# Optimization experiments

Hardware: AMD Instinct MI355X
Metric: run time of the kernel (lower is better)

Reference implementation:

```python
import jax, jax.numpy as jnp
import numpy as np

Q, M, KLEN, B = 512, 512, 1024, 4
D, H, DH, G = 1024, 16, 64, 4
DG = D // G          # 256
EPS = 1e-6
SCALE = 1.0 / DH ** 0.5


def _group_ln(x, gamma, beta, n_group):
    # x: [L, B, D]; torch std is unbiased (ddof=1); note (x-mean)/(std+eps)
    L, b, d = x.shape
    xg = x.reshape(L, b, n_group, d // n_group)
    mean = xg.mean(-1, keepdims=True)
    std = jnp.std(xg, axis=-1, ddof=1, keepdims=True)
    out = ((xg - mean) / (std + EPS)).reshape(L, b, d)
    return gamma * out + beta


def _rel_shift(x):
    # x: [q, r, b, n]
    q, r = x.shape[0], x.shape[1]
    zero_pad = jnp.zeros((q, 1) + x.shape[2:], x.dtype)
    x_padded = jnp.concatenate([zero_pad, x], axis=1).reshape((r + 1, q) + x.shape[2:])
    return x_padded[1:].reshape(x.shape)


def setup_inputs() -> dict:
    key = jax.random.key(0)
    ks = jax.random.split(key, 14)
    p = lambda k, s: jax.random.normal(k, s, jnp.float32) * 0.02
    w = jax.random.normal(ks[0], (Q, B, D), jnp.float32)
    r = jax.random.normal(ks[1], (KLEN, 1, D), jnp.float32)
    mems = jax.random.normal(ks[2], (M, B, D), jnp.float32)
    r_w_bias = p(ks[3], (H, DH))
    r_r_bias = p(ks[4], (H, DH))
    gamma_q = jnp.ones((D,), jnp.float32); beta_q = jnp.zeros((D,), jnp.float32)
    gamma_kv = jnp.ones((D,), jnp.float32); beta_kv = jnp.zeros((D,), jnp.float32)
    Wq = p(ks[5], (G, DG, DG))       # grouped conv1d k=1: per-group [out,in]
    Wiq = p(ks[6], (DG, D))          # inter_q_net: conv1d groups=1 [out,in]
    Wk = p(ks[7], (D, D))
    Wv = p(ks[8], (D, D))
    Wr = p(ks[9], (G, DG, DG))       # r_net grouped (n_head*d_head == d_model)
    Wintra = p(ks[10], (G, DG, DG))  # intra_linear grouped conv
    Winter = p(ks[11], (DG, D))      # inter_linear nn.Linear weight
    i = jnp.arange(Q)[:, None]
    j = jnp.arange(KLEN)[None, :]
    attn_mask = (j > i + M)[:, :, None]  # [Q, KLEN, 1] bool, True = masked
    return dict(w=w, r=r, r_w_bias=r_w_bias, r_r_bias=r_r_bias, mems=mems,
                gamma_q=gamma_q, beta_q=beta_q, gamma_kv=gamma_kv, beta_kv=beta_kv,
                Wq=Wq, Wiq=Wiq, Wk=Wk, Wv=Wv, Wr=Wr, Wintra=Wintra, Winter=Winter,
                attn_mask=attn_mask)


def reference(w, r, r_w_bias, r_r_bias, mems, gamma_q, beta_q, gamma_kv, beta_kv,
              Wq, Wiq, Wk, Wv, Wr, Wintra, Winter, attn_mask):
    qlen, bsz, _ = w.shape
    rlen = r.shape[0]
    w_norm = _group_ln(w, gamma_q, beta_q, G)                       # [Q,B,D]
    kv = jnp.concatenate([mems, w], axis=0)
    kv_norm = gamma_kv * (kv - kv.mean(-1, keepdims=True)) / (
        jnp.std(kv, axis=-1, ddof=1, keepdims=True) + EPS) + beta_kv  # [K,B,D]

    # grouped 1x1 conv projections == per-group matmuls
    q_intra = jnp.einsum('qbgd,god->qbgo', w_norm.reshape(qlen, bsz, G, DG), Wq)
    q_global = jnp.einsum('qbd,od->qbo', w_norm, Wiq)               # [Q,B,DG]
    head_q = (q_intra + q_global[:, :, None, :]).reshape(qlen, bsz, H, DH)
    klen = kv_norm.shape[0]
    head_k = jnp.einsum('kbd,od->kbo', kv_norm, Wk).reshape(klen, bsz, H, DH)
    head_v = jnp.einsum('kbd,od->kbo', kv_norm, Wv).reshape(klen, bsz, H, DH)
    r_head_k = jnp.einsum('rgd,god->rgo', r[:, 0].reshape(rlen, G, DG), Wr)
    r_head_k = r_head_k.reshape(rlen, H, DH)                        # [R,H,DH]

    AC = jnp.einsum('ibnd,jbnd->ijbn', head_q + r_w_bias, head_k)
    BD = _rel_shift(jnp.einsum('ibnd,jnd->ijbn', head_q + r_r_bias, r_head_k))
    attn_score = (AC + BD) * SCALE                                  # [Q,K,B,H]
    attn_score = jnp.where(attn_mask[:, :, :, None], -jnp.inf, attn_score)
    attn_prob = jax.nn.softmax(attn_score, axis=1)
    attn_vec = jnp.einsum('ijbn,jbnd->ibnd', attn_prob, head_v)
    attn_out = attn_vec.reshape(qlen, bsz, D)

    inter = jnp.einsum('qbd,od->qbo', attn_out, Winter)             # [Q,B,DG]
    intra = jnp.einsum('qbgd,god->qbgo', attn_out.reshape(qlen, bsz, G, DG), Wintra)
    out = (intra + inter[:, :, None, :]).reshape(qlen, bsz, D)
    return w + out
```

## Files before the change

kernel.cpp:

```cpp
#include <hip/hip_runtime.h>
#include <math.h>

#define Q_LEN 512
#define M_LEN 512
#define KL    1024
#define BSZ   4
#define DM    1024
#define NH    16
#define DHD   64
#define NG    4
#define DGRP  256
#define RL    1024
#define LN_EPS 1e-6f
#define ATT_SCALE 0.125f

typedef short s16x8 __attribute__((ext_vector_type(8)));
typedef float f32x4 __attribute__((ext_vector_type(4)));

__device__ __forceinline__ float wave_sum64(float v) {
#pragma unroll
    for (int off = 32; off > 0; off >>= 1) v += __shfl_xor(v, off);
    return v;
}

__device__ __forceinline__ ushort f2bf(float f) {
    unsigned u = __float_as_uint(f);
    unsigned r = (u + 0x7fffu + ((u >> 16) & 1u)) >> 16;
    return (ushort)r;
}
__device__ __forceinline__ float bf2f(ushort u) {
    return __uint_as_float(((unsigned)u) << 16);
}

__global__ __launch_bounds__(256) void prep_kernel(
    const float* __restrict__ r, const float* __restrict__ Wk,
    const float* __restrict__ Wv, const float* __restrict__ Wr,
    const float* __restrict__ Wq, const float* __restrict__ Wiq,
    const float* __restrict__ Wintra, const float* __restrict__ Winter,
    ushort* __restrict__ r_bf, ushort* __restrict__ Wk_bf,
    ushort* __restrict__ Wv_bf, ushort* __restrict__ Wr_bf,
    ushort* __restrict__ Wq_aug, ushort* __restrict__ Wo_aug)
{
    int bid = blockIdx.x;
    if (bid < 3328) {
        const float* s; ushort* d; int off;
        if      (bid < 1024) { s = r;  d = r_bf;  off = bid; }
        else if (bid < 2048) { s = Wk; d = Wk_bf; off = bid - 1024; }
        else if (bid < 3072) { s = Wv; d = Wv_bf; off = bid - 2048; }
        else                 { s = Wr; d = Wr_bf; off = bid - 3072; }
        int i = off * 1024 + threadIdx.x * 4;
        float4 v = *(const float4*)(s + i);
        ushort4 o;
        o.x = f2bf(v.x); o.y = f2bf(v.y); o.z = f2bf(v.z); o.w = f2bf(v.w);
        *(ushort4*)(d + i) = o;
    } else {
        const float* Wg; const float* Wf; ushort* Wo; int off;
        if (bid < 4352) { Wg = Wq;     Wf = Wiq;    Wo = Wq_aug; off = bid - 3328; }
        else            { Wg = Wintra; Wf = Winter; Wo = Wo_aug; off = bid - 4352; }
        int idx = off * 1024 + threadIdx.x * 4;
        int g = idx >> 18;
        int o = (idx >> 10) & 255;
        int k = idx & 1023;
        float4 v = *(const float4*)(Wf + o * 1024 + k);
        if ((k >> 8) == g) {
            float4 vg = *(const float4*)(Wg + ((g * 256 + o) << 8) + (k & 255));
            v.x += vg.x; v.y += vg.y; v.z += vg.z; v.w += vg.w;
        }
        ushort4 u;
        u.x = f2bf(v.x); u.y = f2bf(v.y); u.z = f2bf(v.z); u.w = f2bf(v.w);
        *(ushort4*)(Wo + idx) = u;
    }
}

__global__ __launch_bounds__(64) void group_ln_kernel(
    const float* __restrict__ w, const float* __restrict__ gamma,
    const float* __restrict__ beta, ushort* __restrict__ out)
{
    int bid = blockIdx.x;
    int g = bid & (NG - 1);
    long long row = bid >> 2;
    int t = threadIdx.x;
    long long base = row * DM + g * DGRP + t * 4;
    float4 x = *(const float4*)(w + base);
    float mean = wave_sum64(x.x + x.y + x.z + x.w) * (1.0f / 256.0f);
    float dx = x.x - mean, dy = x.y - mean, dz = x.z - mean, dw = x.w - mean;
    float ss = wave_sum64(dx * dx + dy * dy + dz * dz + dw * dw);
    float inv = 1.0f / (sqrtf(ss * (1.0f / 255.0f)) + LN_EPS);
    int db = g * DGRP + t * 4;
    float4 ga = *(const float4*)(gamma + db);
    float4 be = *(const float4*)(beta + db);
    ushort4 o;
    o.x = f2bf(ga.x * (dx * inv) + be.x);
    o.y = f2bf(ga.y * (dy * inv) + be.y);
    o.z = f2bf(ga.z * (dz * inv) + be.z);
    o.w = f2bf(ga.w * (dw * inv) + be.w);
    *(ushort4*)(out + base) = o;
}

__global__ __launch_bounds__(256) void kv_ln_kernel(
    const float* __restrict__ mems, const float* __restrict__ w,
    const float* __restrict__ gamma, const float* __restrict__ beta,
    ushort* __restrict__ out)
{
    int row = blockIdx.x;
    int k = row >> 2, b = row & 3;
    const float* src = (k < M_LEN) ? (mems + ((long long)k * BSZ + b) * DM)
                                   : (w + ((long long)(k - M_LEN) * BSZ + b) * DM);
    int t = threadIdx.x;
    float4 x = *(const float4*)(src + t * 4);
    __shared__ float red[4];
    float s = wave_sum64(x.x + x.y + x.z + x.w);
    int wv = t >> 6, ln = t & 63;
    if (ln == 0) red[wv] = s;
    __syncthreads();
    float mean = (red[0] + red[1] + red[2] + red[3]) * (1.0f / 1024.0f);
    float dx = x.x - mean, dy = x.y - mean, dz = x.z - mean, dw = x.w - mean;
    float ss = wave_sum64(dx * dx + dy * dy + dz * dz + dw * dw);
    __syncthreads();
    if (ln == 0) red[wv] = ss;
    __syncthreads();
    float var = (red[0] + red[1] + red[2] + red[3]) * (1.0f / 1023.0f);
    float inv = 1.0f / (sqrtf(var) + LN_EPS);
    int db = t * 4;
    float4 ga = *(const float4*)(gamma + db);
    float4 be = *(const float4*)(beta + db);
    ushort4 o;
    o.x = f2bf(ga.x * (dx * inv) + be.x);
    o.y = f2bf(ga.y * (dy * inv) + be.y);
    o.z = f2bf(ga.z * (dz * inv) + be.z);
    o.w = f2bf(ga.w * (dw * inv) + be.w);
    *(ushort4*)(out + (long long)row * DM + db) = o;
}

__global__ __launch_bounds__(256) void gemm128_bf16_nt(
    const ushort* __restrict__ A, int lda,
    const ushort* __restrict__ W, long long wZ, int ldw,
    ushort* __restrict__ Cb, long long cZ, int ldc, int K)
{
    int z = blockIdx.z;
    W += (long long)z * wZ;
    Cb += (long long)z * cZ;
    int m0 = blockIdx.y * 128, n0 = blockIdx.x * 128;
    int t = threadIdx.x, lane = t & 63, w = t >> 6;
    int wr = w >> 1, wc = w & 1;
    int fr = lane & 15, kq = (lane >> 4) * 8;
    int srow = t >> 1, scol = (t & 1) * 16;

    __shared__ __align__(16) ushort As[128][40];
    __shared__ __align__(16) ushort Ws[128][40];

    const ushort* Ar = A + (long long)(m0 + srow) * lda + scol;
    const ushort* Wr = W + (long long)(n0 + srow) * ldw + scol;

    f32x4 acc[16] = {};

    s16x8 a0 = *(const s16x8*)Ar, a1 = *(const s16x8*)(Ar + 8);
    s16x8 b0 = *(const s16x8*)Wr, b1 = *(const s16x8*)(Wr + 8);
    *(s16x8*)&As[srow][scol] = a0; *(s16x8*)&As[srow][scol + 8] = a1;
    *(s16x8*)&Ws[srow][scol] = b0; *(s16x8*)&Ws[srow][scol + 8] = b1;
    __syncthreads();

    for (int k0 = 0; k0 < K; k0 += 32) {
        bool more = (k0 + 32) < K;
        if (more) {
            a0 = *(const s16x8*)(Ar + k0 + 32); a1 = *(const s16x8*)(Ar + k0 + 40);
            b0 = *(const s16x8*)(Wr + k0 + 32); b1 = *(const s16x8*)(Wr + k0 + 40);
        }
        s16x8 af[4], bf_[4];
#pragma unroll
        for (int rb = 0; rb < 4; ++rb)
            af[rb] = *(const s16x8*)&As[wr * 64 + rb * 16 + fr][kq];
#pragma unroll
        for (int cb = 0; cb < 4; ++cb)
            bf_[cb] = *(const s16x8*)&Ws[wc * 64 + cb * 16 + fr][kq];
#pragma unroll
        for (int rb = 0; rb < 4; ++rb)
#pragma unroll
            for (int cb = 0; cb < 4; ++cb)
                acc[rb * 4 + cb] = __builtin_amdgcn_mfma_f32_16x16x32_bf16(
                    af[rb], bf_[cb], acc[rb * 4 + cb], 0, 0, 0);
        __syncthreads();
        if (more) {
            *(s16x8*)&As[srow][scol] = a0; *(s16x8*)&As[srow][scol + 8] = a1;
            *(s16x8*)&Ws[srow][scol] = b0; *(s16x8*)&Ws[srow][scol + 8] = b1;
            __syncthreads();
        }
    }

    int rbase = (lane >> 4) * 4;
#pragma unroll
    for (int rb = 0; rb < 4; ++rb)
#pragma unroll
        for (int p = 0; p < 4; ++p) {
            long long row = m0 + wr * 64 + rb * 16 + rbase + p;
            ushort* crow = Cb + row * ldc + n0 + wc * 64 + fr;
#pragma unroll
            for (int cb = 0; cb < 4; ++cb)
                crow[cb * 16] = f2bf(acc[rb * 4 + cb][p]);
        }
}

__global__ __launch_bounds__(256) void gemm_bf16_nt(
    const ushort* __restrict__ A, long long aZ, int lda,
    const ushort* __restrict__ W, long long wZ, int ldw,
    float* __restrict__ C, ushort* __restrict__ Cb, long long cZ, int ldc,
    int M, int N, int K,
    const float* __restrict__ add1, long long a1Z, int lda1,
    const float* __restrict__ add2, long long a2Z, int lda2)
{
    int z = blockIdx.z;
    A += (long long)z * aZ;
    W += (long long)z * wZ;
    if (C)  C += (long long)z * cZ;
    if (Cb) Cb += (long long)z * cZ;
    if (add1) add1 += (long long)z * a1Z;
    if (add2) add2 += (long long)z * a2Z;
    int m0 = blockIdx.y * 64, n0 = blockIdx.x * 64;
    int t = threadIdx.x;
    int lane = t & 63, wid = t >> 6;
    int wr = wid >> 1, wc = wid & 1;
    int srow = t >> 2, scol = (t & 3) * 16;
    int fr = lane & 15, kq = (lane >> 4) * 8;

    __shared__ __align__(16) ushort As[64][72];
    __shared__ __align__(16) ushort Ws[64][72];

    f32x4 acc00 = {}, acc01 = {}, acc10 = {}, acc11 = {};

    const ushort* Arow = A + (long long)(m0 + srow) * lda + scol;
    const ushort* Wrow = W + (long long)(n0 + srow) * ldw + scol;

    s16x8 ra0 = *(const s16x8*)Arow;
    s16x8 ra1 = *(const s16x8*)(Arow + 8);
    s16x8 rw0 = *(const s16x8*)Wrow;
    s16x8 rw1 = *(const s16x8*)(Wrow + 8);
    *(s16x8*)&As[srow][scol] = ra0; *(s16x8*)&As[srow][scol + 8] = ra1;
    *(s16x8*)&Ws[srow][scol] = rw0; *(s16x8*)&Ws[srow][scol + 8] = rw1;
    __syncthreads();

    for (int k0 = 0; k0 < K; k0 += 64) {
        bool hasNext = (k0 + 64) < K;
        if (hasNext) {
            ra0 = *(const s16x8*)(Arow + k0 + 64);
            ra1 = *(const s16x8*)(Arow + k0 + 72);
            rw0 = *(const s16x8*)(Wrow + k0 + 64);
            rw1 = *(const s16x8*)(Wrow + k0 + 72);
        }
#pragma unroll
        for (int kk = 0; kk < 64; kk += 32) {
            s16x8 a0 = *(const s16x8*)&As[wr * 32 + fr][kk + kq];
            s16x8 a1 = *(const s16x8*)&As[wr * 32 + 16 + fr][kk + kq];
            s16x8 b0 = *(const s16x8*)&Ws[wc * 32 + fr][kk + kq];
            s16x8 b1 = *(const s16x8*)&Ws[wc * 32 + 16 + fr][kk + kq];
            acc00 = __builtin_amdgcn_mfma_f32_16x16x32_bf16(a0, b0, acc00, 0, 0, 0);
            acc01 = __builtin_amdgcn_mfma_f32_16x16x32_bf16(a0, b1, acc01, 0, 0, 0);
            acc10 = __builtin_amdgcn_mfma_f32_16x16x32_bf16(a1, b0, acc10, 0, 0, 0);
            acc11 = __builtin_amdgcn_mfma_f32_16x16x32_bf16(a1, b1, acc11, 0, 0, 0);
        }
        __syncthreads();
        if (hasNext) {
            *(s16x8*)&As[srow][scol] = ra0; *(s16x8*)&As[srow][scol + 8] = ra1;
            *(s16x8*)&Ws[srow][scol] = rw0; *(s16x8*)&Ws[srow][scol + 8] = rw1;
            __syncthreads();
        }
    }

    int rbase = (lane >> 4) * 4;
#pragma unroll
    for (int p = 0; p < 4; ++p) {
        int mrow0 = wr * 32 + rbase + p;
        int mrow1 = mrow0 + 16;
        int ncol0 = wc * 32 + fr;
        int ncol1 = ncol0 + 16;
        float v00 = acc00[p], v01 = acc01[p], v10 = acc10[p], v11 = acc11[p];
        long long r0 = m0 + mrow0, r1 = m0 + mrow1;
        int c0 = n0 + ncol0, c1 = n0 + ncol1;
        if (add1) {
            v00 += add1[r0 * lda1 + c0]; v01 += add1[r0 * lda1 + c1];
            v10 += add1[r1 * lda1 + c0]; v11 += add1[r1 * lda1 + c1];
        }
        if (add2) {
            v00 += add2[r0 * lda2 + c0]; v01 += add2[r0 * lda2 + c1];
            v10 += add2[r1 * lda2 + c0]; v11 += add2[r1 * lda2 + c1];
        }
        if (Cb) {
            Cb[r0 * ldc + c0] = f2bf(v00); Cb[r0 * ldc + c1] = f2bf(v01);
            Cb[r1 * ldc + c0] = f2bf(v10); Cb[r1 * ldc + c1] = f2bf(v11);
        } else {
            C[r0 * ldc + c0] = v00; C[r0 * ldc + c1] = v01;
            C[r1 * ldc + c0] = v10; C[r1 * ldc + c1] = v11;
        }
    }
}

__global__ __launch_bounds__(256) void transpose_v_kernel(
    const ushort* __restrict__ vin, ushort* __restrict__ vout)
{
    __shared__ __align__(16) ushort T[64][72];
    int bn = blockIdx.y;
    int b = bn >> 4, n = bn & 15;
    int k0 = blockIdx.x * 64;
    int t = threadIdx.x;
    {
        int kr = t >> 2, dp = (t & 3) * 16;
        const ushort* sp = vin + (((long long)(k0 + kr)) * 4 + b) * DM + n * DHD + dp;
        *(s16x8*)&T[kr][dp] = *(const s16x8*)sp;
        *(s16x8*)&T[kr][dp + 8] = *(const s16x8*)(sp + 8);
    }
    __syncthreads();
    {
        int d = t >> 2, kp = (t & 3) * 16;
        ushort vals[16];
#pragma unroll
        for (int q = 0; q < 16; ++q) vals[q] = T[kp + q][d];
        ushort* dp = vout + ((long long)bn * DHD + d) * KL + k0 + kp;
        *(s16x8*)dp = *(const s16x8*)&vals[0];
        *(s16x8*)(dp + 8) = *(const s16x8*)&vals[8];
    }
}

__global__ __launch_bounds__(256) void corr_kernel(
    const ushort* __restrict__ r_hk, const float* __restrict__ rwb,
    const float* __restrict__ rrb, float* __restrict__ corr)
{
    int n = blockIdx.y;
    int k = blockIdx.x * 4 + (threadIdx.x >> 6);
    int d = threadIdx.x & 63;
    float diff = rrb[n * DHD + d] - rwb[n * DHD + d];
    float v = diff * bf2f(r_hk[(long long)k * DM + n * DHD + d]);
    v = wave_sum64(v);
    if (d == 0) corr[n * RL + k] = v;
}

__global__ __launch_bounds__(256) void attn_mfma_kernel(
    const ushort* __restrict__ hq, const ushort* __restrict__ hk,
    const ushort* __restrict__ hvT, const ushort* __restrict__ rhk,
    const float* __restrict__ corr, ushort* __restrict__ attn_out)
{
    __shared__ __align__(16) ushort Ks[2][64][72];
    __shared__ __align__(16) ushort VsT[2][64][72];
    __shared__ __align__(16) ushort RKs[128][72];
    __shared__ __align__(16) ushort BDs[64][128];
    __shared__ __align__(16) ushort Ps[64][64];

    int bh = blockIdx.y;
    int b = bh >> 4, n = bh & 15;
    int xb = blockIdx.x;
    if (bh >= 32) xb = 7 - xb;
    int i0 = xb * 64;
    int t = threadIdx.x;
    int lane = t & 63, w = t >> 6;
    int lr16 = lane & 15;
    int lk8 = (lane >> 4) * 8;
    int orow = (lane >> 4) * 4;
    int swzBD = ((lane >> 4) & 3) << 4;

    s16x8 qf0, qf1;
    {
        const ushort* qp = hq + (((long long)(i0 + w * 16 + lr16)) * 4 + b) * DM
                              + n * DHD + lk8;
        qf0 = *(const s16x8*)qp;
        qf1 = *(const s16x8*)(qp + 32);
    }

    f32x4 O[4] = {};
    float m_[4], l_[4];
#pragma unroll
    for (int r = 0; r < 4; ++r) { m_[r] = -INFINITY; l_[r] = 0.0f; }

    int nJ = ((i0 + 575) >> 6) + 1;
    if (nJ > 16) nJ = 16;
    int ka0 = 448 - i0;

    int srow = t >> 2, sdp = (t & 3) * 16;

    {
        const ushort* kp = hk + (((long long)srow) * 4 + b) * DM + n * DHD + sdp;
        *(s16x8*)&Ks[0][srow][sdp] = *(const s16x8*)kp;
        *(s16x8*)&Ks[0][srow][sdp + 8] = *(const s16x8*)(kp + 8);
        const ushort* vp = hvT + ((long long)bh * DHD + srow) * KL + sdp;
        *(s16x8*)&VsT[0][srow][sdp] = *(const s16x8*)vp;
        *(s16x8*)&VsT[0][srow][sdp + 8] = *(const s16x8*)(vp + 8);
        int rr = t >> 1, dp2 = (t & 1) * 32;
        int rabs = ka0 + rr;
        const ushort* rp = rhk + (long long)rabs * DM + n * DHD + dp2;
        int phys = rabs & 127;
#pragma unroll
        for (int q = 0; q < 4; ++q)
            *(s16x8*)&RKs[phys][dp2 + q * 8] = *(const s16x8*)(rp + q * 8);
    }
    __syncthreads();

    int cur = 0;
    for (int jt = 0; jt < nJ; ++jt) {
        int j0 = jt * 64;
        int ka = ka0 + j0;
        bool hasNext = (jt + 1) < nJ;

        s16x8 pk0 = {}, pk1 = {}, pv0 = {}, pv1 = {}, pr0 = {}, pr1 = {};
        if (hasNext) {
            int j0n = j0 + 64;
            const ushort* kp = hk + (((long long)(j0n + srow)) * 4 + b) * DM + n * DHD + sdp;
            pk0 = *(const s16x8*)kp;
            pk1 = *(const s16x8*)(kp + 8);
            const ushort* vp = hvT + ((long long)bh * DHD + srow) * KL + j0n + sdp;
            pv0 = *(const s16x8*)vp;
            pv1 = *(const s16x8*)(vp + 8);
            int rnew = ka + 128 + srow;
            if (rnew < RL) {
                const ushort* rp = rhk + (long long)rnew * DM + n * DHD + sdp;
                pr0 = *(const s16x8*)rp;
                pr1 = *(const s16x8*)(rp + 8);
            }
        }

        __builtin_amdgcn_s_setprio(1);
        f32x4 ac[4] = {};
#pragma unroll
        for (int nb = 0; nb < 4; ++nb) {
            s16x8 kb0 = *(const s16x8*)&Ks[cur][nb * 16 + lr16][lk8];
            s16x8 kb1 = *(const s16x8*)&Ks[cur][nb * 16 + lr16][32 + lk8];
            ac[nb] = __builtin_amdgcn_mfma_f32_16x16x32_bf16(qf0, kb0, ac[nb], 0, 0, 0);
            ac[nb] = __builtin_amdgcn_mfma_f32_16x16x32_bf16(qf1, kb1, ac[nb], 0, 0, 0);
        }
        int nb0 = (jt == 0) ? 0 : 4;
        for (int nb = nb0; nb < 8; ++nb) {
            int kk = nb * 16 + lr16;
            int rabs = ka + kk;
            int phys = rabs & 127;
            f32x4 bd = {};
            s16x8 rb0 = *(const s16x8*)&RKs[phys][lk8];
            s16x8 rb1 = *(const s16x8*)&RKs[phys][32 + lk8];
            bd = __builtin_amdgcn_mfma_f32_16x16x32_bf16(qf0, rb0, bd, 0, 0, 0);
            bd = __builtin_amdgcn_mfma_f32_16x16x32_bf16(qf1, rb1, bd, 0, 0, 0);
            float cadd = (rabs < RL) ? corr[n * RL + rabs] : 0.0f;
            int colw = phys ^ swzBD;
#pragma unroll
            for (int reg = 0; reg < 4; ++reg)
                BDs[w * 16 + orow + reg][colw] = f2bf(bd[reg] + cadd);
        }
        __builtin_amdgcn_s_setprio(0);
        if (jt == 0) __syncthreads();

        float pvv[4][4], rowm[4];
#pragma unroll
        for (int reg = 0; reg < 4; ++reg) {
            int il = w * 16 + orow + reg;
            int i = i0 + il;
            rowm[reg] = -INFINITY;
#pragma unroll
            for (int nb = 0; nb < 4; ++nb) {
                int jc = nb * 16 + lr16;
                int j = j0 + jc;
                float s = -INFINITY;
                if (j <= i + M_LEN) {
                    int phys = (j + 511 - i) & 127;
                    s = (ac[nb][reg] + bf2f(BDs[il][phys ^ swzBD])) * ATT_SCALE;
                }
                pvv[reg][nb] = s;
                rowm[reg] = fmaxf(rowm[reg], s);
            }
        }
#pragma unroll
        for (int st = 1; st <= 8; st <<= 1)
#pragma unroll
            for (int reg = 0; reg < 4; ++reg)
                rowm[reg] = fmaxf(rowm[reg], __shfl_xor(rowm[reg], st));
        float rs[4], alpha[4];
#pragma unroll
        for (int reg = 0; reg < 4; ++reg) {
            int il = w * 16 + orow + reg;
            float newm = fmaxf(m_[reg], rowm[reg]);
            alpha[reg] = __expf(m_[reg] - newm);
            m_[reg] = newm;
            rs[reg] = 0.0f;
#pragma unroll
            for (int nb = 0; nb < 4; ++nb) {
                float p = __expf(pvv[reg][nb] - newm);
                rs[reg] += p;
                int jc = nb * 16 + lr16;
                int colp = (((jc >> 3) ^ (il & 7)) << 3) | (jc & 7);
                Ps[il][colp] = f2bf(p);
            }
        }
#pragma unroll
        for (int st = 1; st <= 8; st <<= 1)
#pragma unroll
            for (int reg = 0; reg < 4; ++reg)
                rs[reg] += __shfl_xor(rs[reg], st);
#pragma unroll
        for (int reg = 0; reg < 4; ++reg) {
            l_[reg] = l_[reg] * alpha[reg] + rs[reg];
#pragma unroll
            for (int nb = 0; nb < 4; ++nb) O[nb][reg] *= alpha[reg];
        }

        {
            int prow = w * 16 + lr16;
            int rh = prow & 7;
            __builtin_amdgcn_s_setprio(1);
#pragma unroll
            for (int kc = 0; kc < 2; ++kc) {
                int blk = kc * 4 + (lane >> 4);
                s16x8 pa = *(const s16x8*)&Ps[prow][(blk ^ rh) << 3];
#pragma unroll
                for (int nb = 0; nb < 4; ++nb) {
                    s16x8 vb = *(const s16x8*)&VsT[cur][nb * 16 + lr16][kc * 32 + lk8];
                    O[nb] = __builtin_amdgcn_mfma_f32_16x16x32_bf16(pa, vb, O[nb], 0, 0, 0);
                }
            }
            __builtin_amdgcn_s_setprio(0);
        }

        if (hasNext) {
            *(s16x8*)&Ks[cur ^ 1][srow][sdp] = pk0;
            *(s16x8*)&Ks[cur ^ 1][srow][sdp + 8] = pk1;
            *(s16x8*)&VsT[cur ^ 1][srow][sdp] = pv0;
            *(s16x8*)&VsT[cur ^ 1][srow][sdp + 8] = pv1;
            int phys = (ka + 128 + srow) & 127;
            *(s16x8*)&RKs[phys][sdp] = pr0;
            *(s16x8*)&RKs[phys][sdp + 8] = pr1;
        }
        __syncthreads();
        cur ^= 1;
    }

#pragma unroll
    for (int reg = 0; reg < 4; ++reg) {
        int il = w * 16 + orow + reg;
        long long i = i0 + il;
        float inv = 1.0f / l_[reg];
#pragma unroll
        for (int nb = 0; nb < 4; ++nb)
            attn_out[(i * 4 + b) * DM + n * DHD + nb * 16 + lr16] = f2bf(O[nb][reg] * inv);
    }
}

extern "C" void kernel_launch(void* const* d_in, const int* in_sizes, int n_in,
                              void* d_out, int out_size, void* d_ws, size_t ws_size,
                              hipStream_t stream) {
    const float* w       = (const float*)d_in[0];
    const float* r       = (const float*)d_in[1];
    const float* rwb     = (const float*)d_in[2];
    const float* rrb     = (const float*)d_in[3];
    const float* mems    = (const float*)d_in[4];
    const float* gamma_q = (const float*)d_in[5];
    const float* beta_q  = (const float*)d_in[6];
    const float* gamma_kv= (const float*)d_in[7];
    const float* beta_kv = (const float*)d_in[8];
    const float* Wq      = (const float*)d_in[9];
    const float* Wiq     = (const float*)d_in[10];
    const float* Wk      = (const float*)d_in[11];
    const float* Wv      = (const float*)d_in[12];
    const float* Wr      = (const float*)d_in[13];
    const float* Wintra  = (const float*)d_in[14];
    const float* Winter  = (const float*)d_in[15];
    float* out = (float*)d_out;
    float* ws = (float*)d_ws;

    float* corr = ws;

    ushort* w_norm_bf  = (ushort*)(corr + 16384);
    ushort* kv_norm_bf = w_norm_bf + 2097152;
    ushort* head_q_bf  = kv_norm_bf + 4194304;
    ushort* head_k_bf  = head_q_bf + 2097152;
    ushort* head_v_bf  = head_k_bf + 4194304;
    ushort* head_vT_bf = head_v_bf + 4194304;
    ushort* r_hk_bf    = head_vT_bf + 4194304;
    ushort* attn_o_bf  = r_hk_bf + 1048576;
    ushort* r_bf       = attn_o_bf + 2097152;
    ushort* Wk_bf      = r_bf + 1048576;
    ushort* Wv_bf      = Wk_bf + 1048576;
    ushort* Wr_bf      = Wv_bf + 1048576;
    ushort* Wq_aug     = Wr_bf + 262144;
    ushort* Wo_aug     = Wq_aug + 1048576;

    group_ln_kernel<<<dim3(Q_LEN * BSZ * NG), 64, 0, stream>>>(w, gamma_q, beta_q, w_norm_bf);
    kv_ln_kernel<<<dim3(KL * BSZ), 256, 0, stream>>>(mems, w, gamma_kv, beta_kv, kv_norm_bf);

    prep_kernel<<<dim3(5376), 256, 0, stream>>>(
        r, Wk, Wv, Wr, Wq, Wiq, Wintra, Winter,
        r_bf, Wk_bf, Wv_bf, Wr_bf, Wq_aug, Wo_aug);

    gemm128_bf16_nt<<<dim3(8, 32, 2), 256, 0, stream>>>(
        kv_norm_bf, DM, Wk_bf, 1048576, DM, head_k_bf, 4194304, DM, DM);
    transpose_v_kernel<<<dim3(16, 64), 256, 0, stream>>>(head_v_bf, head_vT_bf);

    gemm_bf16_nt<<<dim3(4, 32, 4), 256, 0, stream>>>(
        w_norm_bf, 0, DM, Wq_aug, 262144, DM, nullptr, head_q_bf, DGRP, DM,
        Q_LEN * BSZ, DGRP, DM, nullptr, 0, 0, rwb, DGRP, 0);
    gemm_bf16_nt<<<dim3(4, 16, 4), 256, 0, stream>>>(
        r_bf, DGRP, DM, Wr_bf, DGRP * DGRP, DGRP, nullptr, r_hk_bf, DGRP, DM,
        RL, DGRP, DGRP, nullptr, 0, 0, nullptr, 0, 0);

    corr_kernel<<<dim3(RL / 4, NH), 256, 0, stream>>>(r_hk_bf, rwb, rrb, corr);

    attn_mfma_kernel<<<dim3(Q_LEN / 64, BSZ * NH), 256, 0, stream>>>(
        head_q_bf, head_k_bf, head_vT_bf, r_hk_bf, corr, attn_o_bf);

    gemm_bf16_nt<<<dim3(4, 32, 4), 256, 0, stream>>>(
        attn_o_bf, 0, DM, Wo_aug, 262144, DM, out, nullptr, DGRP, DM,
        Q_LEN * BSZ, DGRP, DM, w, DGRP, DM, nullptr, 0, 0);
}
```

Before: 163.0 us.

## Merge LN kernels and batch K/V/Q/R projections into one multi-GEMM launch

The grouped and full-row layer norms now run as one combined launch. The grouped r projection weight is expanded into a zero-padded block-diagonal 1024x1024 matrix, so it can share the 128-tile GEMM. The K, V, Q and R projections then run in a single gemm128_multi launch indexed by blockIdx.z, with the Q bias applied in the epilogue. This removes several kernel launches and lets small GEMMs fill the GPU together, at the cost of extra FLOPs on the zero blocks of the r weight and some empty blocks that exit early.

```diff
diff --git a/kernel.cpp b/kernel.cpp
--- a/kernel.cpp
+++ b/kernel.cpp
@@ -32,31 +32,100 @@
     return __uint_as_float(((unsigned)u) << 16);
 }
 
+__global__ __launch_bounds__(256) void ln_kernel(
+    const float* __restrict__ w, const float* __restrict__ mems,
+    const float* __restrict__ gamma_q, const float* __restrict__ beta_q,
+    const float* __restrict__ gamma_kv, const float* __restrict__ beta_kv,
+    ushort* __restrict__ w_norm, ushort* __restrict__ kv_norm)
+{
+    int bid = blockIdx.x;
+    int t = threadIdx.x;
+    if (bid < 2048) {
+        long long row = bid;
+        int g = t >> 6, ln = t & 63;
+        long long base = row * DM + g * DGRP + ln * 4;
+        float4 x = *(const float4*)(w + base);
+        float mean = wave_sum64(x.x + x.y + x.z + x.w) * (1.0f / 256.0f);
+        float dx = x.x - mean, dy = x.y - mean, dz = x.z - mean, dw_ = x.w - mean;
+        float ss = wave_sum64(dx * dx + dy * dy + dz * dz + dw_ * dw_);
+        float inv = 1.0f / (sqrtf(ss * (1.0f / 255.0f)) + LN_EPS);
+        int db = g * DGRP + ln * 4;
+        float4 ga = *(const float4*)(gamma_q + db);
+        float4 be = *(const float4*)(beta_q + db);
+        ushort4 o;
+        o.x = f2bf(ga.x * (dx * inv) + be.x);
+        o.y = f2bf(ga.y * (dy * inv) + be.y);
+        o.z = f2bf(ga.z * (dz * inv) + be.z);
+        o.w = f2bf(ga.w * (dw_ * inv) + be.w);
+        *(ushort4*)(w_norm + base) = o;
+    } else {
+        int row = bid - 2048;
+        int k = row >> 2, b = row & 3;
+        const float* src = (k < M_LEN) ? (mems + ((long long)k * BSZ + b) * DM)
+                                       : (w + ((long long)(k - M_LEN) * BSZ + b) * DM);
+        float4 x = *(const float4*)(src + t * 4);
+        __shared__ float red[4];
+        float s = wave_sum64(x.x + x.y + x.z + x.w);
+        int wv = t >> 6, ln = t & 63;
+        if (ln == 0) red[wv] = s;
+        __syncthreads();
+        float mean = (red[0] + red[1] + red[2] + red[3]) * (1.0f / 1024.0f);
+        float dx = x.x - mean, dy = x.y - mean, dz = x.z - mean, dw_ = x.w - mean;
+        float ss = wave_sum64(dx * dx + dy * dy + dz * dz + dw_ * dw_);
+        __syncthreads();
+        if (ln == 0) red[wv] = ss;
+        __syncthreads();
+        float var = (red[0] + red[1] + red[2] + red[3]) * (1.0f / 1023.0f);
+        float inv = 1.0f / (sqrtf(var) + LN_EPS);
+        int db = t * 4;
+        float4 ga = *(const float4*)(gamma_kv + db);
+        float4 be = *(const float4*)(beta_kv + db);
+        ushort4 o;
+        o.x = f2bf(ga.x * (dx * inv) + be.x);
+        o.y = f2bf(ga.y * (dy * inv) + be.y);
+        o.z = f2bf(ga.z * (dz * inv) + be.z);
+        o.w = f2bf(ga.w * (dw_ * inv) + be.w);
+        *(ushort4*)(kv_norm + (long long)row * DM + db) = o;
+    }
+}
+
 __global__ __launch_bounds__(256) void prep_kernel(
     const float* __restrict__ r, const float* __restrict__ Wk,
     const float* __restrict__ Wv, const float* __restrict__ Wr,
     const float* __restrict__ Wq, const float* __restrict__ Wiq,
     const float* __restrict__ Wintra, const float* __restrict__ Winter,
     ushort* __restrict__ r_bf, ushort* __restrict__ Wk_bf,
-    ushort* __restrict__ Wv_bf, ushort* __restrict__ Wr_bf,
+    ushort* __restrict__ Wv_bf, ushort* __restrict__ Wr_diag,
     ushort* __restrict__ Wq_aug, ushort* __restrict__ Wo_aug)
 {
     int bid = blockIdx.x;
-    if (bid < 3328) {
+    if (bid < 3072) {
         const float* s; ushort* d; int off;
         if      (bid < 1024) { s = r;  d = r_bf;  off = bid; }
         else if (bid < 2048) { s = Wk; d = Wk_bf; off = bid - 1024; }
-        else if (bid < 3072) { s = Wv; d = Wv_bf; off = bid - 2048; }
-        else                 { s = Wr; d = Wr_bf; off = bid - 3072; }
+        else                 { s = Wv; d = Wv_bf; off = bid - 2048; }
         int i = off * 1024 + threadIdx.x * 4;
         float4 v = *(const float4*)(s + i);
         ushort4 o;
         o.x = f2bf(v.x); o.y = f2bf(v.y); o.z = f2bf(v.z); o.w = f2bf(v.w);
         *(ushort4*)(d + i) = o;
+    } else if (bid < 4096) {
+        int idx = (bid - 3072) * 1024 + threadIdx.x * 4;
+        int row = idx >> 10;
+        int k = idx & 1023;
+        int g = row >> 8;
+        ushort4 u;
+        if ((k >> 8) == g) {
+            float4 v = *(const float4*)(Wr + (row << 8) + (k & 255));
+            u.x = f2bf(v.x); u.y = f2bf(v.y); u.z = f2bf(v.z); u.w = f2bf(v.w);
+        } else {
+            u.x = 0; u.y = 0; u.z = 0; u.w = 0;
+        }
+        *(ushort4*)(Wr_diag + idx) = u;
     } else {
         const float* Wg; const float* Wf; ushort* Wo; int off;
-        if (bid < 4352) { Wg = Wq;     Wf = Wiq;    Wo = Wq_aug; off = bid - 3328; }
-        else            { Wg = Wintra; Wf = Winter; Wo = Wo_aug; off = bid - 4352; }
+        if (bid < 5120) { Wg = Wq;     Wf = Wiq;    Wo = Wq_aug; off = bid - 4096; }
+        else            { Wg = Wintra; Wf = Winter; Wo = Wo_aug; off = bid - 5120; }
         int idx = off * 1024 + threadIdx.x * 4;
         int g = idx >> 18;
         int o = (idx >> 10) & 255;
@@ -72,74 +141,24 @@
     }
 }
 
-__global__ __launch_bounds__(64) void group_ln_kernel(
-    const float* __restrict__ w, const float* __restrict__ gamma,
-    const float* __restrict__ beta, ushort* __restrict__ out)
-{
-    int bid = blockIdx.x;
-    int g = bid & (NG - 1);
-    long long row = bid >> 2;
-    int t = threadIdx.x;
-    long long base = row * DM + g * DGRP + t * 4;
-    float4 x = *(const float4*)(w + base);
-    float mean = wave_sum64(x.x + x.y + x.z + x.w) * (1.0f / 256.0f);
-    float dx = x.x - mean, dy = x.y - mean, dz = x.z - mean, dw = x.w - mean;
-    float ss = wave_sum64(dx * dx + dy * dy + dz * dz + dw * dw);
-    float inv = 1.0f / (sqrtf(ss * (1.0f / 255.0f)) + LN_EPS);
-    int db = g * DGRP + t * 4;
-    float4 ga = *(const float4*)(gamma + db);
-    float4 be = *(const float4*)(beta + db);
-    ushort4 o;
-    o.x = f2bf(ga.x * (dx * inv) + be.x);
-    o.y = f2bf(ga.y * (dy * inv) + be.y);
-    o.z = f2bf(ga.z * (dz * inv) + be.z);
-    o.w = f2bf(ga.w * (dw * inv) + be.w);
-    *(ushort4*)(out + base) = o;
-}
-
-__global__ __launch_bounds__(256) void kv_ln_kernel(
-    const float* __restrict__ mems, const float* __restrict__ w,
-    const float* __restrict__ gamma, const float* __restrict__ beta,
-    ushort* __restrict__ out)
-{
-    int row = blockIdx.x;
-    int k = row >> 2, b = row & 3;
-    const float* src = (k < M_LEN) ? (mems + ((long long)k * BSZ + b) * DM)
-                                   : (w + ((long long)(k - M_LEN) * BSZ + b) * DM);
-    int t = threadIdx.x;
-    float4 x = *(const float4*)(src + t * 4);
-    __shared__ float red[4];
-    float s = wave_sum64(x.x + x.y + x.z + x.w);
-    int wv = t >> 6, ln = t & 63;
-    if (ln == 0) red[wv] = s;
-    __syncthreads();
-    float mean = (red[0] + red[1] + red[2] + red[3]) * (1.0f / 1024.0f);
-    float dx = x.x - mean, dy = x.y - mean, dz = x.z - mean, dw = x.w - mean;
-    float ss = wave_sum64(dx * dx + dy * dy + dz * dz + dw * dw);
-    __syncthreads();
-    if (ln == 0) red[wv] = ss;
-    __syncthreads();
-    float var = (red[0] + red[1] + red[2] + red[3]) * (1.0f / 1023.0f);
-    float inv = 1.0f / (sqrtf(var) + LN_EPS);
-    int db = t * 4;
-    float4 ga = *(const float4*)(gamma + db);
-    float4 be = *(const float4*)(beta + db);
-    ushort4 o;
-    o.x = f2bf(ga.x * (dx * inv) + be.x);
-    o.y = f2bf(ga.y * (dy * inv) + be.y);
-    o.z = f2bf(ga.z * (dz * inv) + be.z);
-    o.w = f2bf(ga.w * (dw * inv) + be.w);
-    *(ushort4*)(out + (long long)row * DM + db) = o;
-}
-
-__global__ __launch_bounds__(256) void gemm128_bf16_nt(
-    const ushort* __restrict__ A, int lda,
-    const ushort* __restrict__ W, long long wZ, int ldw,
-    ushort* __restrict__ Cb, long long cZ, int ldc, int K)
+__global__ __launch_bounds__(256) void gemm128_multi(
+    const ushort* __restrict__ A0, const ushort* __restrict__ A1,
+    const ushort* __restrict__ A2, const ushort* __restrict__ A3,
+    int y0, int y1, int y2, int y3,
+    const ushort* __restrict__ W0, const ushort* __restrict__ W1,
+    const ushort* __restrict__ W2, const ushort* __restrict__ W3,
+    ushort* __restrict__ C0, ushort* __restrict__ C1,
+    ushort* __restrict__ C2, ushort* __restrict__ C3,
+    const float* __restrict__ bias2)
 {
     int z = blockIdx.z;
-    W += (long long)z * wZ;
-    Cb += (long long)z * cZ;
+    const ushort* A; const ushort* W; ushort* Cb; const float* bias = nullptr; int yMax;
+    if      (z == 0) { A = A0; W = W0; Cb = C0; yMax = y0; }
+    else if (z == 1) { A = A1; W = W1; Cb = C1; yMax = y1; }
+    else if (z == 2) { A = A2; W = W2; Cb = C2; yMax = y2; bias = bias2; }
+    else             { A = A3; W = W3; Cb = C3; yMax = y3; }
+    if (blockIdx.y >= yMax) return;
+
     int m0 = blockIdx.y * 128, n0 = blockIdx.x * 128;
     int t = threadIdx.x, lane = t & 63, w = t >> 6;
     int wr = w >> 1, wc = w & 1;
@@ -149,22 +168,22 @@
     __shared__ __align__(16) ushort As[128][40];
     __shared__ __align__(16) ushort Ws[128][40];
 
-    const ushort* Ar = A + (long long)(m0 + srow) * lda + scol;
-    const ushort* Wr = W + (long long)(n0 + srow) * ldw + scol;
+    const ushort* Ar = A + (long long)(m0 + srow) * DM + scol;
+    const ushort* Wrp = W + (long long)(n0 + srow) * DM + scol;
 
     f32x4 acc[16] = {};
 
     s16x8 a0 = *(const s16x8*)Ar, a1 = *(const s16x8*)(Ar + 8);
-    s16x8 b0 = *(const s16x8*)Wr, b1 = *(const s16x8*)(Wr + 8);
+    s16x8 b0 = *(const s16x8*)Wrp, b1 = *(const s16x8*)(Wrp + 8);
     *(s16x8*)&As[srow][scol] = a0; *(s16x8*)&As[srow][scol + 8] = a1;
     *(s16x8*)&Ws[srow][scol] = b0; *(s16x8*)&Ws[srow][scol + 8] = b1;
     __syncthreads();
 
-    for (int k0 = 0; k0 < K; k0 += 32) {
-        bool more = (k0 + 32) < K;
+    for (int k0 = 0; k0 < DM; k0 += 32) {
+        bool more = (k0 + 32) < DM;
         if (more) {
             a0 = *(const s16x8*)(Ar + k0 + 32); a1 = *(const s16x8*)(Ar + k0 + 40);
-            b0 = *(const s16x8*)(Wr + k0 + 32); b1 = *(const s16x8*)(Wr + k0 + 40);
+            b0 = *(const s16x8*)(Wrp + k0 + 32); b1 = *(const s16x8*)(Wrp + k0 + 40);
         }
         s16x8 af[4], bf_[4];
 #pragma unroll
@@ -193,10 +212,13 @@
 #pragma unroll
         for (int p = 0; p < 4; ++p) {
             long long row = m0 + wr * 64 + rb * 16 + rbase + p;
-            ushort* crow = Cb + row * ldc + n0 + wc * 64 + fr;
-#pragma unroll
-            for (int cb = 0; cb < 4; ++cb)
-                crow[cb * 16] = f2bf(acc[rb * 4 + cb][p]);
+            ushort* crow = Cb + row * DM + n0 + wc * 64 + fr;
+#pragma unroll
+            for (int cb = 0; cb < 4; ++cb) {
+                float v = acc[rb * 4 + cb][p];
+                if (bias) v += bias[n0 + wc * 64 + cb * 16 + fr];
+                crow[cb * 16] = f2bf(v);
+            }
         }
 }
 
@@ -571,27 +593,25 @@
     ushort* r_bf       = attn_o_bf + 2097152;
     ushort* Wk_bf      = r_bf + 1048576;
     ushort* Wv_bf      = Wk_bf + 1048576;
-    ushort* Wr_bf      = Wv_bf + 1048576;
-    ushort* Wq_aug     = Wr_bf + 262144;
+    ushort* Wr_diag    = Wv_bf + 1048576;
+    ushort* Wq_aug     = Wr_diag + 1048576;
     ushort* Wo_aug     = Wq_aug + 1048576;
 
-    group_ln_kernel<<<dim3(Q_LEN * BSZ * NG), 64, 0, stream>>>(w, gamma_q, beta_q, w_norm_bf);
-    kv_ln_kernel<<<dim3(KL * BSZ), 256, 0, stream>>>(mems, w, gamma_kv, beta_kv, kv_norm_bf);
-
-    prep_kernel<<<dim3(5376), 256, 0, stream>>>(
+    ln_kernel<<<dim3(6144), 256, 0, stream>>>(
+        w, mems, gamma_q, beta_q, gamma_kv, beta_kv, w_norm_bf, kv_norm_bf);
+
+    prep_kernel<<<dim3(6144), 256, 0, stream>>>(
         r, Wk, Wv, Wr, Wq, Wiq, Wintra, Winter,
-        r_bf, Wk_bf, Wv_bf, Wr_bf, Wq_aug, Wo_aug);
-
-    gemm128_bf16_nt<<<dim3(8, 32, 2), 256, 0, stream>>>(
-        kv_norm_bf, DM, Wk_bf, 1048576, DM, head_k_bf, 4194304, DM, DM);
+        r_bf, Wk_bf, Wv_bf, Wr_diag, Wq_aug, Wo_aug);
+
+    gemm128_multi<<<dim3(8, 32, 4), 256, 0, stream>>>(
+        kv_norm_bf, kv_norm_bf, w_norm_bf, r_bf,
+        32, 32, 16, 8,
+        Wk_bf, Wv_bf, Wq_aug, Wr_diag,
+        head_k_bf, head_v_bf, head_q_bf, r_hk_bf,
+        rwb);
+
     transpose_v_kernel<<<dim3(16, 64), 256, 0, stream>>>(head_v_bf, head_vT_bf);
-
-    gemm_bf16_nt<<<dim3(4, 32, 4), 256, 0, stream>>>(
-        w_norm_bf, 0, DM, Wq_aug, 262144, DM, nullptr, head_q_bf, DGRP, DM,
-        Q_LEN * BSZ, DGRP, DM, nullptr, 0, 0, rwb, DGRP, 0);
-    gemm_bf16_nt<<<dim3(4, 16, 4), 256, 0, stream>>>(
-        r_bf, DGRP, DM, Wr_bf, DGRP * DGRP, DGRP, nullptr, r_hk_bf, DGRP, DM,
-        RL, DGRP, DGRP, nullptr, 0, 0, nullptr, 0, 0);
 
     corr_kernel<<<dim3(RL / 4, NH), 256, 0, stream>>>(r_hk_bf, rwb, rrb, corr);
 
```

Measured after the change: 167.5 us. 1.03x slower.
